# Kernel optimization log

Hardware: AMD Instinct MI355X
Metric: run time of the kernel (lower is better)

The kernel has to match this reference:

```python
import jax, jax.numpy as jnp
import numpy as np

D_MODEL, EXPAND, D_STATE, D_CONV, HEADDIM = 1024, 2, 64, 4, 64
D_INNER = EXPAND * D_MODEL          # 2048
NHEADS = D_INNER // HEADDIM         # 32
CONV_DIM = D_INNER + 2 * D_STATE    # x, B, C go through the depthwise conv
D_IN_PROJ = 2 * D_INNER + 2 * D_STATE + NHEADS  # z, xBC, dt
EPS = 1e-5


def setup_inputs() -> dict:
    key = jax.random.key(0)
    ks = jax.random.split(key, 16)
    s = 0.02
    inp = {
        "x": jax.random.normal(ks[0], (2, 2048, D_MODEL), jnp.float32),
        "ln1_w": jnp.ones((D_MODEL,), jnp.float32),
        "ln1_b": jnp.zeros((D_MODEL,), jnp.float32),
        "in_proj_w": jax.random.normal(ks[1], (D_IN_PROJ, D_MODEL), jnp.float32) * s,
        "conv_w": jax.random.normal(ks[2], (CONV_DIM, D_CONV), jnp.float32) * 0.3,
        "conv_b": jnp.zeros((CONV_DIM,), jnp.float32),
        # dt_bias so that softplus(dt+dt_bias) lands in ~[1e-3, 0.1] (mamba2 init)
        "dt_bias": jnp.log(jnp.expm1(jnp.exp(jax.random.uniform(ks[3], (NHEADS,), jnp.float32, jnp.log(1e-3), jnp.log(0.1))))),
        "A_log": jnp.log(jax.random.uniform(ks[4], (NHEADS,), jnp.float32, 1.0, 16.0)),
        "D": jnp.ones((NHEADS,), jnp.float32),
        "norm_w": jnp.ones((D_INNER,), jnp.float32),
        "out_proj_w": jax.random.normal(ks[5], (D_MODEL, D_INNER), jnp.float32) * s,
        "ln2_w": jnp.ones((D_MODEL,), jnp.float32),
        "ln2_b": jnp.zeros((D_MODEL,), jnp.float32),
        "mlp_w1": jax.random.normal(ks[6], (4 * D_MODEL, D_MODEL), jnp.float32) * s,
        "mlp_b1": jnp.zeros((4 * D_MODEL,), jnp.float32),
        "mlp_w2": jax.random.normal(ks[7], (D_MODEL, 4 * D_MODEL), jnp.float32) * s,
        "mlp_b2": jnp.zeros((D_MODEL,), jnp.float32),
    }
    return inp


def _layernorm(x, w, b):
    mu = jnp.mean(x, axis=-1, keepdims=True)
    var = jnp.mean(jnp.square(x - mu), axis=-1, keepdims=True)
    return (x - mu) * jax.lax.rsqrt(var + EPS) * w + b


def _mamba2(x, in_proj_w, conv_w, conv_b, dt_bias, A_log, D, norm_w, out_proj_w):
    Bt, L, _ = x.shape
    zxbcdt = x @ in_proj_w.T                                  # [B,L,D_IN_PROJ]
    z = zxbcdt[..., :D_INNER]
    xBC = zxbcdt[..., D_INNER:D_INNER + CONV_DIM]
    dt = jax.nn.softplus(zxbcdt[..., D_INNER + CONV_DIM:] + dt_bias)  # [B,L,H]
    # causal depthwise conv1d, kernel D_CONV, then SiLU
    xp = jnp.pad(xBC, ((0, 0), (D_CONV - 1, 0), (0, 0)))
    conv = conv_b
    for k in range(D_CONV):
        conv = conv + xp[:, k:k + L, :] * conv_w[:, k]
    xBC = jax.nn.silu(conv)
    xs = xBC[..., :D_INNER].reshape(Bt, L, NHEADS, HEADDIM)   # [B,L,H,P]
    Bm = xBC[..., D_INNER:D_INNER + D_STATE]                  # [B,L,N] (ngroups=1)
    Cm = xBC[..., D_INNER + D_STATE:]                         # [B,L,N]
    A = -jnp.exp(A_log)                                       # [H]

    def step(h, inp):
        x_t, dt_t, B_t, C_t = inp                             # [B,H,P],[B,H],[B,N],[B,N]
        dA = jnp.exp(dt_t * A)                                # [B,H]
        h = h * dA[:, :, None, None] + (dt_t[:, :, None] * x_t)[..., None] * B_t[:, None, None, :]
        y = jnp.einsum('bhpn,bn->bhp', h, C_t)
        return h, y

    h0 = jnp.zeros((Bt, NHEADS, HEADDIM, D_STATE), x.dtype)
    xsT = jnp.moveaxis(xs, 1, 0)
    dtT = jnp.moveaxis(dt, 1, 0)
    BT = jnp.moveaxis(Bm, 1, 0)
    CT = jnp.moveaxis(Cm, 1, 0)
    _, ys = jax.lax.scan(step, h0, (xsT, dtT, BT, CT))        # ys: [L,B,H,P]
    y = jnp.moveaxis(ys, 0, 1) + xs * D[None, None, :, None]  # skip D
    y = y.reshape(Bt, L, D_INNER)
    # gated RMSNorm: rmsnorm(y * silu(z)) * norm_w
    y = y * jax.nn.silu(z)
    y = y * jax.lax.rsqrt(jnp.mean(jnp.square(y), axis=-1, keepdims=True) + EPS) * norm_w
    return y @ out_proj_w.T


def reference(x, ln1_w, ln1_b, in_proj_w, conv_w, conv_b, dt_bias, A_log, D,
              norm_w, out_proj_w, ln2_w, ln2_b, mlp_w1, mlp_b1, mlp_w2, mlp_b2):
    res = x
    h = _layernorm(x, ln1_w, ln1_b)
    h = _mamba2(h, in_proj_w, conv_w, conv_b, dt_bias, A_log, D, norm_w, out_proj_w)
    x = res + h
    res = x
    h = _layernorm(x, ln2_w, ln2_b)
    h = jax.nn.gelu(h @ mlp_w1.T + mlp_b1, approximate=False) @ mlp_w2.T + mlp_b2
    return res + h
```

## Files before the change

kernel.cpp:

```cpp
#include <hip/hip_runtime.h>
#include <hip/hip_bf16.h>
#include <math.h>

using bf16 = __hip_bfloat16;
typedef __attribute__((ext_vector_type(8))) short short8;
typedef __attribute__((ext_vector_type(4))) float floatx4;

#define SEQLEN   2048
#define ROWS     4096
#define DMODEL   1024
#define DINNER   2048
#define NHEADS   32
#define HEADDIM  64
#define DSTATE   64
#define CONVDIM  2176
#define DINPROJ  4256
#define NCHUNK   32

__device__ __forceinline__ float b2f(bf16 x) { return __bfloat162float(x); }
__device__ __forceinline__ bf16  f2b(float x) { return __float2bfloat16(x); }
__device__ __forceinline__ float s2f(short s) { union { short s; bf16 b; } u; u.s = s; return b2f(u.b); }
__device__ __forceinline__ short f2s(float f) { union { short s; bf16 b; } u; u.b = f2b(f); return u.s; }

typedef __attribute__((address_space(1))) void v_as1;
typedef __attribute__((address_space(3))) void v_as3;
__device__ __forceinline__ void gload_lds16(const void* g, void* l) {
  __builtin_amdgcn_global_load_lds((v_as1*)(g), (v_as3*)(l), 16, 0, 0);
}

__global__ void cvt_kernel(const float* __restrict__ in, bf16* __restrict__ out, int n4) {
  int i = blockIdx.x * 256 + threadIdx.x;
  if (i < n4) {
    float4 v = ((const float4*)in)[i];
    union { bf16 h[4]; uint2 u; } r;
    r.h[0] = f2b(v.x); r.h[1] = f2b(v.y); r.h[2] = f2b(v.z); r.h[3] = f2b(v.w);
    ((uint2*)out)[i] = r.u;
  }
}

__device__ __forceinline__ void block_reduce_2(float& a, float& b) {
#pragma unroll
  for (int off = 32; off > 0; off >>= 1) {
    a += __shfl_xor(a, off);
    b += __shfl_xor(b, off);
  }
  __shared__ float ra[4], rb[4];
  int w = threadIdx.x >> 6;
  if ((threadIdx.x & 63) == 0) { ra[w] = a; rb[w] = b; }
  __syncthreads();
  a = ra[0] + ra[1] + ra[2] + ra[3];
  b = rb[0] + rb[1] + rb[2] + rb[3];
}

__global__ void ln_kernel(const float* __restrict__ x, const float* __restrict__ w,
                          const float* __restrict__ b, bf16* __restrict__ out)
{
  int row = blockIdx.x;
  int tid = threadIdx.x;
  float v[4]; float s = 0.f, sq = 0.f;
#pragma unroll
  for (int k = 0; k < 4; ++k) {
    int c = k * 256 + tid;
    float xv = x[(size_t)row * DMODEL + c];
    v[k] = xv; s += xv; sq += xv * xv;
  }
  block_reduce_2(s, sq);
  float mu  = s * (1.f / DMODEL);
  float var = sq * (1.f / DMODEL) - mu * mu;
  float rs  = rsqrtf(var + 1e-5f);
#pragma unroll
  for (int k = 0; k < 4; ++k) {
    int c = k * 256 + tid;
    out[(size_t)row * DMODEL + c] = f2b((v[k] - mu) * rs * w[c] + b[c]);
  }
}

template<int EPI>
__global__ __launch_bounds__(256, 2)
void gemm_bt(const bf16* __restrict__ A, const bf16* __restrict__ W,
             const float* __restrict__ bias, const float* __restrict__ resid,
             void* __restrict__ Cout, int M, int N, int K)
{
  __shared__ __align__(16) short Asl[128 * 64];
  __shared__ __align__(16) short Bsl[128 * 64];
  const int tid  = threadIdx.x;
  const int lane = tid & 63;
  const int wv   = tid >> 6;
  const int wm   = wv >> 1, wn = wv & 1;
  const int r16  = lane & 15, q = lane >> 4;
  const int m0   = blockIdx.y * 128;
  const int n0   = blockIdx.x * 128;

  floatx4 acc[4][4] = {};

  for (int k0 = 0; k0 < K; k0 += 64) {
#pragma unroll
    for (int it = 0; it < 4; ++it) {
      int idx = it * 256 + tid;
      int row = m0 + (idx >> 3);
      int cb  = (idx & 7) << 3;
      gload_lds16(A + (size_t)row * K + k0 + cb, &Asl[idx * 8]);
    }
#pragma unroll
    for (int it = 0; it < 4; ++it) {
      int idx = it * 256 + tid;
      int row = n0 + (idx >> 3);
      if (row > N - 1) row = N - 1;
      int cb  = (idx & 7) << 3;
      gload_lds16(W + (size_t)row * K + k0 + cb, &Bsl[idx * 8]);
    }
    __syncthreads();
#pragma unroll
    for (int kk = 0; kk < 64; kk += 32) {
      short8 af[4], bfr[4];
#pragma unroll
      for (int i = 0; i < 4; ++i)
        af[i] = *(const short8*)&Asl[(wm * 64 + i * 16 + r16) * 64 + kk + q * 8];
#pragma unroll
      for (int j = 0; j < 4; ++j)
        bfr[j] = *(const short8*)&Bsl[(wn * 64 + j * 16 + r16) * 64 + kk + q * 8];
#pragma unroll
      for (int i = 0; i < 4; ++i)
#pragma unroll
        for (int j = 0; j < 4; ++j)
          acc[i][j] = __builtin_amdgcn_mfma_f32_16x16x32_bf16(af[i], bfr[j], acc[i][j], 0, 0, 0);
    }
    __syncthreads();
  }

#pragma unroll
  for (int i = 0; i < 4; ++i) {
#pragma unroll
    for (int j = 0; j < 4; ++j) {
#pragma unroll
      for (int r = 0; r < 4; ++r) {
        int row = m0 + wm * 64 + i * 16 + q * 4 + r;
        int col = n0 + wn * 64 + j * 16 + r16;
        if (col < N) {
          float v = acc[i][j][r];
          size_t off = (size_t)row * N + col;
          if (EPI == 0) {
            ((bf16*)Cout)[off] = f2b(v);
          } else if (EPI == 1) {
            v += bias[col];
            v = 0.5f * v * (1.f + erff(v * 0.70710678118654752f));
            ((bf16*)Cout)[off] = f2b(v);
          } else if (EPI == 2) {
            v += resid[off];
            ((float*)Cout)[off] = v;
          } else {
            v += bias[col] + resid[off];
            ((float*)Cout)[off] = v;
          }
        }
      }
    }
  }
}

__global__ void conv_kernel(const bf16* __restrict__ zx, const float* __restrict__ cw,
                            const float* __restrict__ cb, const float* __restrict__ dtbias,
                            bf16* __restrict__ xbc, bf16* __restrict__ Bb,
                            bf16* __restrict__ Cbb, float* __restrict__ dtb)
{
  int row = blockIdx.x;
  int b = row >> 11, t = row & 2047;
  for (int c = threadIdx.x; c < CONVDIM; c += 256) {
    float acc = cb[c];
#pragma unroll
    for (int k = 0; k < 4; ++k) {
      int tt = t + k - 3;
      if (tt >= 0)
        acc += b2f(zx[((size_t)(b * SEQLEN + tt)) * DINPROJ + DINNER + c]) * cw[c * 4 + k];
    }
    float s = acc / (1.f + __expf(-acc));
    xbc[(size_t)row * CONVDIM + c] = f2b(s);
    if (c >= DINNER) {
      if (c < DINNER + DSTATE) Bb[row * DSTATE + (c - DINNER)] = f2b(s);
      else                     Cbb[row * DSTATE + (c - DINNER - DSTATE)] = f2b(s);
    }
  }
  if (threadIdx.x < NHEADS) {
    int hh = threadIdx.x;
    float raw = b2f(zx[(size_t)row * DINPROJ + DINNER + CONVDIM + hh]) + dtbias[hh];
    float dt = raw > 20.f ? raw : log1pf(__expf(raw));
    dtb[row * NHEADS + hh] = dt;
  }
}

__device__ __forceinline__ float wave_incl_prefix(float a, int lane) {
#pragma unroll
  for (int off = 1; off < 64; off <<= 1) {
    float o = __shfl_up(a, off);
    if (lane >= off) a += o;
  }
  return a;
}

__global__ __launch_bounds__(64)
void chunk_state_kernel(const bf16* __restrict__ xbc, const bf16* __restrict__ Bb,
                        const float* __restrict__ dtb, const float* __restrict__ A_log,
                        float* __restrict__ Sbuf, float* __restrict__ Pbuf)
{
  const int blk = blockIdx.x;
  const int c = blk & 31, h = (blk >> 5) & 31, b = blk >> 10;
  const int bh = b * 32 + h;
  const int lane = threadIdx.x;
  const int row = b * SEQLEN + c * 64 + lane;
  const float Ah = -__expf(A_log[h]);

  float dts = dtb[row * NHEADS + h];
  float E = wave_incl_prefix(dts * Ah, lane);
  float EQ = __shfl(E, 63);
  float w = __expf(EQ - E) * dts;
  if (lane == 63) Pbuf[bh * NCHUNK + c] = __expf(EQ);

  __shared__ __align__(16) short XwT[64 * 72];
  __shared__ __align__(16) short BT[64 * 72];

  const bf16* xrow = xbc + (size_t)row * CONVDIM + h * 64;
  const bf16* brow = Bb + (size_t)row * DSTATE;
#pragma unroll
  for (int i = 0; i < 8; ++i) {
    short8 xv = *(const short8*)(xrow + i * 8);
    short8 bv = *(const short8*)(brow + i * 8);
#pragma unroll
    for (int j = 0; j < 8; ++j) {
      XwT[(i * 8 + j) * 72 + lane] = f2s(w * s2f(xv[j]));
      BT[(i * 8 + j) * 72 + lane]  = bv[j];
    }
  }
  __syncthreads();

  const int r16 = lane & 15, q = lane >> 4;
  floatx4 acc[4][4] = {};
#pragma unroll
  for (int kk = 0; kk < 64; kk += 32) {
    short8 af[4], bfr[4];
#pragma unroll
    for (int i = 0; i < 4; ++i) af[i]  = *(const short8*)&XwT[(i * 16 + r16) * 72 + kk + q * 8];
#pragma unroll
    for (int j = 0; j < 4; ++j) bfr[j] = *(const short8*)&BT[(j * 16 + r16) * 72 + kk + q * 8];
#pragma unroll
    for (int i = 0; i < 4; ++i)
#pragma unroll
      for (int j = 0; j < 4; ++j)
        acc[i][j] = __builtin_amdgcn_mfma_f32_16x16x32_bf16(af[i], bfr[j], acc[i][j], 0, 0, 0);
  }
  float* Sout = Sbuf + (size_t)(bh * NCHUNK + c) * 4096;
#pragma unroll
  for (int i = 0; i < 4; ++i)
#pragma unroll
    for (int j = 0; j < 4; ++j)
#pragma unroll
      for (int r = 0; r < 4; ++r)
        Sout[(i * 16 + q * 4 + r) * 64 + (j * 16 + r16)] = acc[i][j][r];
}

__global__ __launch_bounds__(64)
void combine_kernel(const float* __restrict__ Sbuf, const float* __restrict__ Pbuf,
                    bf16* __restrict__ HinB)
{
  const int bh = blockIdx.x >> 2, slab = blockIdx.x & 3;
  const int base = slab * 1024 + threadIdx.x * 16;
  float h[16];
#pragma unroll
  for (int k = 0; k < 16; ++k) h[k] = 0.f;
  for (int c = 0; c < NCHUNK; ++c) {
    size_t off = (size_t)(bh * NCHUNK + c) * 4096 + base;
    union { short s[16]; uint4 q[2]; } pk;
#pragma unroll
    for (int k = 0; k < 16; ++k) pk.s[k] = f2s(h[k]);
    *(uint4*)(HinB + off)     = pk.q[0];
    *(uint4*)(HinB + off + 8) = pk.q[1];
    float P = Pbuf[bh * NCHUNK + c];
    const float4* S4 = (const float4*)(Sbuf + off);
#pragma unroll
    for (int k = 0; k < 4; ++k) {
      float4 s = S4[k];
      h[k*4+0] = h[k*4+0] * P + s.x;
      h[k*4+1] = h[k*4+1] * P + s.y;
      h[k*4+2] = h[k*4+2] * P + s.z;
      h[k*4+3] = h[k*4+3] * P + s.w;
    }
  }
}

__global__ __launch_bounds__(64)
void y_kernel(const bf16* __restrict__ xbc, const bf16* __restrict__ Bb,
              const bf16* __restrict__ Cbb, const float* __restrict__ dtb,
              const bf16* __restrict__ HinB, const float* __restrict__ A_log,
              const float* __restrict__ Dp, float* __restrict__ yout)
{
  const int blk = blockIdx.x;
  const int c = blk & 31, h = (blk >> 5) & 31, b = blk >> 10;
  const int bh = b * 32 + h;
  const int lane = threadIdx.x;
  const int row0 = b * SEQLEN + c * 64;
  const int row = row0 + lane;
  const float Ah = -__expf(A_log[h]);
  const float Dh = Dp[h];

  __shared__ __align__(16) short XdT[64 * 72];
  __shared__ __align__(16) short Msh[64 * 72];
  __shared__ float Esh[64];

  float dts = dtb[row * NHEADS + h];
  float E = wave_incl_prefix(dts * Ah, lane);
  Esh[lane] = E;

  const bf16* xrow = xbc + (size_t)row * CONVDIM + h * 64;
#pragma unroll
  for (int i = 0; i < 8; ++i) {
    short8 xv = *(const short8*)(xrow + i * 8);
#pragma unroll
    for (int j = 0; j < 8; ++j)
      XdT[(i * 8 + j) * 72 + lane] = f2s(dts * s2f(xv[j]));
  }
  __syncthreads();

  const int r16 = lane & 15, q = lane >> 4;

  floatx4 accg[4][4] = {};
#pragma unroll
  for (int kk = 0; kk < 64; kk += 32) {
    short8 af[4], bfr[4];
#pragma unroll
    for (int i = 0; i < 4; ++i)
      af[i]  = *(const short8*)(Cbb + (size_t)(row0 + i * 16 + r16) * DSTATE + kk + q * 8);
#pragma unroll
    for (int j = 0; j < 4; ++j)
      bfr[j] = *(const short8*)(Bb + (size_t)(row0 + j * 16 + r16) * DSTATE + kk + q * 8);
#pragma unroll
    for (int i = 0; i < 4; ++i)
#pragma unroll
      for (int j = 0; j < 4; ++j)
        accg[i][j] = __builtin_amdgcn_mfma_f32_16x16x32_bf16(af[i], bfr[j], accg[i][j], 0, 0, 0);
  }
#pragma unroll
  for (int i = 0; i < 4; ++i)
#pragma unroll
    for (int j = 0; j < 4; ++j)
#pragma unroll
      for (int r = 0; r < 4; ++r) {
        int t = i * 16 + q * 4 + r;
        int s = j * 16 + r16;
        float v = (s <= t) ? __expf(Esh[t] - Esh[s]) * accg[i][j][r] : 0.f;
        Msh[t * 72 + s] = f2s(v);
      }
  __syncthreads();

  floatx4 acc[4][4] = {};
#pragma unroll
  for (int kk = 0; kk < 64; kk += 32) {
    short8 af[4], bfr[4];
#pragma unroll
    for (int i = 0; i < 4; ++i) af[i]  = *(const short8*)&Msh[(i * 16 + r16) * 72 + kk + q * 8];
#pragma unroll
    for (int j = 0; j < 4; ++j) bfr[j] = *(const short8*)&XdT[(j * 16 + r16) * 72 + kk + q * 8];
#pragma unroll
    for (int i = 0; i < 4; ++i)
#pragma unroll
      for (int j = 0; j < 4; ++j)
        acc[i][j] = __builtin_amdgcn_mfma_f32_16x16x32_bf16(af[i], bfr[j], acc[i][j], 0, 0, 0);
  }
  float ei[4];
#pragma unroll
  for (int i = 0; i < 4; ++i) ei[i] = __expf(Esh[i * 16 + r16]);
  const bf16* hinp = HinB + (size_t)(bh * NCHUNK + c) * 4096;
#pragma unroll
  for (int kk = 0; kk < 64; kk += 32) {
    short8 af[4], bfr[4];
#pragma unroll
    for (int i = 0; i < 4; ++i) {
      short8 cv = *(const short8*)(Cbb + (size_t)(row0 + i * 16 + r16) * DSTATE + kk + q * 8);
#pragma unroll
      for (int jj = 0; jj < 8; ++jj) af[i][jj] = f2s(ei[i] * s2f(cv[jj]));
    }
#pragma unroll
    for (int j = 0; j < 4; ++j)
      bfr[j] = *(const short8*)(hinp + (j * 16 + r16) * 64 + kk + q * 8);
#pragma unroll
    for (int i = 0; i < 4; ++i)
#pragma unroll
      for (int j = 0; j < 4; ++j)
        acc[i][j] = __builtin_amdgcn_mfma_f32_16x16x32_bf16(af[i], bfr[j], acc[i][j], 0, 0, 0);
  }
#pragma unroll
  for (int i = 0; i < 4; ++i)
#pragma unroll
    for (int j = 0; j < 4; ++j)
#pragma unroll
      for (int r = 0; r < 4; ++r) {
        int t = i * 16 + q * 4 + r;
        int p = j * 16 + r16;
        int g = row0 + t;
        float y = acc[i][j][r] + Dh * b2f(xbc[(size_t)g * CONVDIM + h * 64 + p]);
        yout[(size_t)g * DINNER + h * 64 + p] = y;
      }
}

__global__ void gate_rms_kernel(const float* __restrict__ y, const bf16* __restrict__ zx,
                                const float* __restrict__ nw, bf16* __restrict__ yn)
{
  int row = blockIdx.x, tid = threadIdx.x;
  float v[8]; float ss = 0.f, dummy = 0.f;
#pragma unroll
  for (int k = 0; k < 8; ++k) {
    int c = k * 256 + tid;
    float z = b2f(zx[(size_t)row * DINPROJ + c]);
    float g = z / (1.f + __expf(-z));
    float val = y[(size_t)row * DINNER + c] * g;
    v[k] = val; ss += val * val;
  }
  block_reduce_2(ss, dummy);
  float rs = rsqrtf(ss * (1.f / DINNER) + 1e-5f);
#pragma unroll
  for (int k = 0; k < 8; ++k) {
    int c = k * 256 + tid;
    yn[(size_t)row * DINNER + c] = f2b(v[k] * rs * nw[c]);
  }
}

extern "C" void kernel_launch(void* const* d_in, const int* in_sizes, int n_in,
                              void* d_out, int out_size, void* d_ws, size_t ws_size,
                              hipStream_t stream)
{
  const float* x         = (const float*)d_in[0];
  const float* ln1_w     = (const float*)d_in[1];
  const float* ln1_b     = (const float*)d_in[2];
  const float* in_proj_w = (const float*)d_in[3];
  const float* conv_w    = (const float*)d_in[4];
  const float* conv_b    = (const float*)d_in[5];
  const float* dt_bias   = (const float*)d_in[6];
  const float* A_log     = (const float*)d_in[7];
  const float* Dp        = (const float*)d_in[8];
  const float* norm_w    = (const float*)d_in[9];
  const float* out_proj_w= (const float*)d_in[10];
  const float* ln2_w     = (const float*)d_in[11];
  const float* ln2_b     = (const float*)d_in[12];
  const float* mlp_w1    = (const float*)d_in[13];
  const float* mlp_b1    = (const float*)d_in[14];
  const float* mlp_w2    = (const float*)d_in[15];
  const float* mlp_b2    = (const float*)d_in[16];

  char* ws = (char*)d_ws;
  bf16*  zx   = (bf16*)(ws + 0);
  bf16*  h1   = (bf16*)(ws + 34865152);
  bf16*  xbc  = (bf16*)(ws + 43253760);
  bf16*  Bb   = (bf16*)(ws + 61079552);
  bf16*  Cbb  = (bf16*)(ws + 61603840);
  float* dtb  = (float*)(ws + 62128128);
  float* Pbuf = (float*)(ws + 62652416);
  float* yw   = (float*)(ws + 62660608);
  bf16*  yn   = (bf16*)(ws + 96215040);
  bf16*  wip  = (bf16*)(ws + 112992256);
  bf16*  wop  = (bf16*)(ws + 121708544);
  float* Sbuf = (float*)(ws + 62660608);
  bf16*  HinB = (bf16*)(ws + 96215040);
  float* x2   = (float*)(ws + 62660608);
  bf16*  h2n  = h1;
  bf16*  mid  = zx;
  bf16*  w1b  = wip;
  bf16*  w2b  = xbc;

  cvt_kernel<<<(4256 * 1024 / 4 + 255) / 256, 256, 0, stream>>>(in_proj_w, wip, 4256 * 1024 / 4);
  ln_kernel<<<ROWS, 256, 0, stream>>>(x, ln1_w, ln1_b, h1);
  gemm_bt<0><<<dim3(34, 32), 256, 0, stream>>>(h1, wip, nullptr, nullptr, zx,
                                               ROWS, DINPROJ, DMODEL);
  cvt_kernel<<<(4096 * 1024 / 4 + 255) / 256, 256, 0, stream>>>(mlp_w1, w1b, 4096 * 1024 / 4);
  cvt_kernel<<<(1024 * 2048 / 4 + 255) / 256, 256, 0, stream>>>(out_proj_w, wop, 1024 * 2048 / 4);
  conv_kernel<<<ROWS, 256, 0, stream>>>(zx, conv_w, conv_b, dt_bias, xbc, Bb, Cbb, dtb);
  chunk_state_kernel<<<2048, 64, 0, stream>>>(xbc, Bb, dtb, A_log, Sbuf, Pbuf);
  combine_kernel<<<256, 64, 0, stream>>>(Sbuf, Pbuf, HinB);
  y_kernel<<<2048, 64, 0, stream>>>(xbc, Bb, Cbb, dtb, HinB, A_log, Dp, yw);
  cvt_kernel<<<(1024 * 4096 / 4 + 255) / 256, 256, 0, stream>>>(mlp_w2, w2b, 1024 * 4096 / 4);
  gate_rms_kernel<<<ROWS, 256, 0, stream>>>(yw, zx, norm_w, yn);
  gemm_bt<2><<<dim3(8, 32), 256, 0, stream>>>(yn, wop, nullptr, x, (void*)x2,
                                              ROWS, DMODEL, DINNER);
  ln_kernel<<<ROWS, 256, 0, stream>>>(x2, ln2_w, ln2_b, h2n);
  gemm_bt<1><<<dim3(32, 32), 256, 0, stream>>>(h2n, w1b, mlp_b1, nullptr, mid,
                                               ROWS, 4 * DMODEL, DMODEL);
  gemm_bt<3><<<dim3(8, 32), 256, 0, stream>>>(mid, w2b, mlp_b2, x2, d_out,
                                              ROWS, DMODEL, 4 * DMODEL);
}
```

Measured before the change: 514.4 us.

## Double-buffer GEMM LDS tiles and store y and residual intermediates in bf16

```diff
diff --git a/kernel.cpp b/kernel.cpp
--- a/kernel.cpp
+++ b/kernel.cpp
@@ -21,6 +21,8 @@
 __device__ __forceinline__ bf16  f2b(float x) { return __float2bfloat16(x); }
 __device__ __forceinline__ float s2f(short s) { union { short s; bf16 b; } u; u.s = s; return b2f(u.b); }
 __device__ __forceinline__ short f2s(float f) { union { short s; bf16 b; } u; u.b = f2b(f); return u.s; }
+__device__ __forceinline__ float tof(float x) { return x; }
+__device__ __forceinline__ float tof(bf16 x)  { return __bfloat162float(x); }
 
 typedef __attribute__((address_space(1))) void v_as1;
 typedef __attribute__((address_space(3))) void v_as3;
@@ -52,7 +54,8 @@
   b = rb[0] + rb[1] + rb[2] + rb[3];
 }
 
-__global__ void ln_kernel(const float* __restrict__ x, const float* __restrict__ w,
+template<typename TIN>
+__global__ void ln_kernel(const TIN* __restrict__ x, const float* __restrict__ w,
                           const float* __restrict__ b, bf16* __restrict__ out)
 {
   int row = blockIdx.x;
@@ -61,7 +64,7 @@
 #pragma unroll
   for (int k = 0; k < 4; ++k) {
     int c = k * 256 + tid;
-    float xv = x[(size_t)row * DMODEL + c];
+    float xv = tof(x[(size_t)row * DMODEL + c]);
     v[k] = xv; s += xv; sq += xv * xv;
   }
   block_reduce_2(s, sq);
@@ -78,11 +81,11 @@
 template<int EPI>
 __global__ __launch_bounds__(256, 2)
 void gemm_bt(const bf16* __restrict__ A, const bf16* __restrict__ W,
-             const float* __restrict__ bias, const float* __restrict__ resid,
+             const float* __restrict__ bias, const void* __restrict__ resid,
              void* __restrict__ Cout, int M, int N, int K)
 {
-  __shared__ __align__(16) short Asl[128 * 64];
-  __shared__ __align__(16) short Bsl[128 * 64];
+  __shared__ __align__(16) short Asl[2][128 * 64];
+  __shared__ __align__(16) short Bsl[2][128 * 64];
   const int tid  = threadIdx.x;
   const int lane = tid & 63;
   const int wv   = tid >> 6;
@@ -90,16 +93,17 @@
   const int r16  = lane & 15, q = lane >> 4;
   const int m0   = blockIdx.y * 128;
   const int n0   = blockIdx.x * 128;
+  const int nk   = K >> 6;
 
   floatx4 acc[4][4] = {};
 
-  for (int k0 = 0; k0 < K; k0 += 64) {
+  auto stage = [&](int buf, int k0) {
 #pragma unroll
     for (int it = 0; it < 4; ++it) {
       int idx = it * 256 + tid;
       int row = m0 + (idx >> 3);
       int cb  = (idx & 7) << 3;
-      gload_lds16(A + (size_t)row * K + k0 + cb, &Asl[idx * 8]);
+      gload_lds16(A + (size_t)row * K + k0 + cb, &Asl[buf][idx * 8]);
     }
 #pragma unroll
     for (int it = 0; it < 4; ++it) {
@@ -107,25 +111,30 @@
       int row = n0 + (idx >> 3);
       if (row > N - 1) row = N - 1;
       int cb  = (idx & 7) << 3;
-      gload_lds16(W + (size_t)row * K + k0 + cb, &Bsl[idx * 8]);
-    }
+      gload_lds16(W + (size_t)row * K + k0 + cb, &Bsl[buf][idx * 8]);
+    }
+  };
+
+  stage(0, 0);
+  for (int k = 0; k < nk; ++k) {
     __syncthreads();
+    if (k + 1 < nk) stage((k + 1) & 1, (k + 1) << 6);
+    const int cur = k & 1;
 #pragma unroll
     for (int kk = 0; kk < 64; kk += 32) {
       short8 af[4], bfr[4];
 #pragma unroll
       for (int i = 0; i < 4; ++i)
-        af[i] = *(const short8*)&Asl[(wm * 64 + i * 16 + r16) * 64 + kk + q * 8];
+        af[i] = *(const short8*)&Asl[cur][(wm * 64 + i * 16 + r16) * 64 + kk + q * 8];
 #pragma unroll
       for (int j = 0; j < 4; ++j)
-        bfr[j] = *(const short8*)&Bsl[(wn * 64 + j * 16 + r16) * 64 + kk + q * 8];
+        bfr[j] = *(const short8*)&Bsl[cur][(wn * 64 + j * 16 + r16) * 64 + kk + q * 8];
 #pragma unroll
       for (int i = 0; i < 4; ++i)
 #pragma unroll
         for (int j = 0; j < 4; ++j)
           acc[i][j] = __builtin_amdgcn_mfma_f32_16x16x32_bf16(af[i], bfr[j], acc[i][j], 0, 0, 0);
     }
-    __syncthreads();
   }
 
 #pragma unroll
@@ -146,10 +155,10 @@
             v = 0.5f * v * (1.f + erff(v * 0.70710678118654752f));
             ((bf16*)Cout)[off] = f2b(v);
           } else if (EPI == 2) {
-            v += resid[off];
-            ((float*)Cout)[off] = v;
+            v += ((const float*)resid)[off];
+            ((bf16*)Cout)[off] = f2b(v);
           } else {
-            v += bias[col] + resid[off];
+            v += bias[col] + b2f(((const bf16*)resid)[off]);
             ((float*)Cout)[off] = v;
           }
         }
@@ -290,7 +299,7 @@
 void y_kernel(const bf16* __restrict__ xbc, const bf16* __restrict__ Bb,
               const bf16* __restrict__ Cbb, const float* __restrict__ dtb,
               const bf16* __restrict__ HinB, const float* __restrict__ A_log,
-              const float* __restrict__ Dp, float* __restrict__ yout)
+              const float* __restrict__ Dp, bf16* __restrict__ yout)
 {
   const int blk = blockIdx.x;
   const int c = blk & 31, h = (blk >> 5) & 31, b = blk >> 10;
@@ -396,11 +405,11 @@
         int p = j * 16 + r16;
         int g = row0 + t;
         float y = acc[i][j][r] + Dh * b2f(xbc[(size_t)g * CONVDIM + h * 64 + p]);
-        yout[(size_t)g * DINNER + h * 64 + p] = y;
+        yout[(size_t)g * DINNER + h * 64 + p] = f2b(y);
       }
 }
 
-__global__ void gate_rms_kernel(const float* __restrict__ y, const bf16* __restrict__ zx,
+__global__ void gate_rms_kernel(const bf16* __restrict__ y, const bf16* __restrict__ zx,
                                 const float* __restrict__ nw, bf16* __restrict__ yn)
 {
   int row = blockIdx.x, tid = threadIdx.x;
@@ -410,7 +419,7 @@
     int c = k * 256 + tid;
     float z = b2f(zx[(size_t)row * DINPROJ + c]);
     float g = z / (1.f + __expf(-z));
-    float val = y[(size_t)row * DINNER + c] * g;
+    float val = b2f(y[(size_t)row * DINNER + c]) * g;
     v[k] = val; ss += val * val;
   }
   block_reduce_2(ss, dummy);
@@ -452,20 +461,20 @@
   bf16*  Cbb  = (bf16*)(ws + 61603840);
   float* dtb  = (float*)(ws + 62128128);
   float* Pbuf = (float*)(ws + 62652416);
-  float* yw   = (float*)(ws + 62660608);
+  float* Sbuf = (float*)(ws + 62660608);
+  bf16*  yw   = (bf16*)(ws + 62660608);
+  bf16*  x2   = (bf16*)(ws + 79437824);
+  bf16*  HinB = (bf16*)(ws + 96215040);
   bf16*  yn   = (bf16*)(ws + 96215040);
   bf16*  wip  = (bf16*)(ws + 112992256);
   bf16*  wop  = (bf16*)(ws + 121708544);
-  float* Sbuf = (float*)(ws + 62660608);
-  bf16*  HinB = (bf16*)(ws + 96215040);
-  float* x2   = (float*)(ws + 62660608);
   bf16*  h2n  = h1;
   bf16*  mid  = zx;
   bf16*  w1b  = wip;
   bf16*  w2b  = xbc;
 
   cvt_kernel<<<(4256 * 1024 / 4 + 255) / 256, 256, 0, stream>>>(in_proj_w, wip, 4256 * 1024 / 4);
-  ln_kernel<<<ROWS, 256, 0, stream>>>(x, ln1_w, ln1_b, h1);
+  ln_kernel<float><<<ROWS, 256, 0, stream>>>(x, ln1_w, ln1_b, h1);
   gemm_bt<0><<<dim3(34, 32), 256, 0, stream>>>(h1, wip, nullptr, nullptr, zx,
                                                ROWS, DINPROJ, DMODEL);
   cvt_kernel<<<(4096 * 1024 / 4 + 255) / 256, 256, 0, stream>>>(mlp_w1, w1b, 4096 * 1024 / 4);
@@ -478,7 +487,7 @@
   gate_rms_kernel<<<ROWS, 256, 0, stream>>>(yw, zx, norm_w, yn);
   gemm_bt<2><<<dim3(8, 32), 256, 0, stream>>>(yn, wop, nullptr, x, (void*)x2,
                                               ROWS, DMODEL, DINNER);
-  ln_kernel<<<ROWS, 256, 0, stream>>>(x2, ln2_w, ln2_b, h2n);
+  ln_kernel<bf16><<<ROWS, 256, 0, stream>>>(x2, ln2_w, ln2_b, h2n);
   gemm_bt<1><<<dim3(32, 32), 256, 0, stream>>>(h2n, w1b, mlp_b1, nullptr, mid,
                                                ROWS, 4 * DMODEL, DMODEL);
   gemm_bt<3><<<dim3(8, 32), 256, 0, stream>>>(mid, w2b, mlp_b2, x2, d_out,
```

Result: slower. 543.9 us (+5.7%).
